# Optimization experiments

Hardware: AMD Instinct MI355X
Metric: run time of the kernel (lower is better)

The kernel has to match this reference:

```python
import jax, jax.numpy as jnp
import numpy as np

N, E, F, EF, D, G = 25000, 100000, 32, 8, 64, 1000


def setup_inputs() -> dict:
    key = jax.random.key(0)
    ks = jax.random.split(key, 32)
    p = lambda k, shape: (jax.random.normal(k, shape, jnp.float32) * 0.05)
    inp = {
        "x": jax.random.normal(ks[0], (N, F), jnp.float32),
        "edge_index": jax.random.randint(ks[1], (2, E), 0, N, jnp.int64 if jax.config.jax_enable_x64 else jnp.int32),
        "edge_attr": jax.random.uniform(ks[2], (E, EF), jnp.float32),
        "batch": jnp.sort(jax.random.randint(ks[3], (N,), 0, G, jnp.int32)),
        # lin0
        "W0": p(ks[4], (F, D)), "b0": p(ks[5], (D,)),
        # edge MLP: Linear(EF, D) -> ReLU -> Linear(D, D*D)
        "We1": p(ks[6], (EF, D)), "be1": p(ks[7], (D,)),
        "We2": p(ks[8], (D, D * D)), "be2": p(ks[9], (D * D,)),
        # NNConv root weight + bias
        "Wroot": p(ks[10], (D, D)), "bconv": p(ks[11], (D,)),
        # GRU (single layer): gate order r, z, n
        "Wi": p(ks[12], (3 * D, D)), "Wh": p(ks[13], (3 * D, D)),
        "bi": p(ks[14], (3 * D,)), "bh": p(ks[15], (3 * D,)),
        # heads
        "W11": p(ks[16], (D, D)), "b11": p(ks[17], (D,)),
        "W12": p(ks[18], (D, D)), "b12": p(ks[19], (D,)),
        "W13": p(ks[20], (D, 1)), "b13": p(ks[21], (1,)),
        "W21": p(ks[22], (D, D)), "b21": p(ks[23], (D,)),
        "W22": p(ks[24], (D, D)), "b22": p(ks[25], (D,)),
        "W23": p(ks[26], (D, 1)), "b23": p(ks[27], (1,)),
    }
    return inp


def reference(x, edge_index, edge_attr, batch,
              W0, b0, We1, be1, We2, be2, Wroot, bconv,
              Wi, Wh, bi, bh,
              W11, b11, W12, b12, W13, b13,
              W21, b21, W22, b22, W23, b23):
    src, dst = edge_index[0], edge_index[1]
    # lin0 + relu
    x1 = jax.nn.relu(x @ W0 + b0)                      # [N, D]
    h = x1                                              # GRU hidden init
    # NNConv: dynamic per-edge weight via edge MLP
    ew = (jax.nn.relu(edge_attr @ We1 + be1) @ We2 + be2).reshape(E, D, D)
    msg = jnp.einsum('ei,eio->eo', x1[src], ew)        # per-edge matmul
    agg = jax.ops.segment_sum(msg, dst, num_segments=N)
    x2 = jax.nn.relu(x1 @ Wroot + agg + bconv)         # [N, D]
    # GRU single step (torch gate order: r, z, n)
    gi = x2 @ Wi.T + bi
    gh = h @ Wh.T + bh
    r = jax.nn.sigmoid(gi[:, :D] + gh[:, :D])
    z = jax.nn.sigmoid(gi[:, D:2 * D] + gh[:, D:2 * D])
    n = jnp.tanh(gi[:, 2 * D:] + r * gh[:, 2 * D:])
    hn = (1.0 - z) * n + z * h                          # [N, D]
    # graph pooling (scatter_add over batch)
    pooled = jax.ops.segment_sum(hn, batch, num_segments=G)  # [G, D]
    # two MLP heads
    x_1 = jax.nn.relu(pooled @ W11 + b11)
    x_1 = jax.nn.relu(x_1 @ W12 + b12)
    x_1 = x_1 @ W13 + b13
    x_2 = jax.nn.relu(pooled @ W21 + b21)
    x_2 = jax.nn.relu(x_2 @ W22 + b22)
    x_2 = x_2 @ W23 + b23
    return jnp.concatenate([x_1, x_2], axis=1)          # [G, 2]
```

## Files before the change

kernel.cpp:

```cpp
#include <hip/hip_runtime.h>
#include <hip/hip_bf16.h>

#define NN 25000
#define NE 100000
#define FIN 32
#define DD 64
#define NG 1000

typedef unsigned short u16;
typedef __attribute__((ext_vector_type(8))) short short8;
typedef __attribute__((ext_vector_type(4))) float f32x4;

__device__ __forceinline__ float b2f(u16 u) {
    union { unsigned int i; float f; } v; v.i = ((unsigned int)u) << 16; return v.f;
}
__device__ __forceinline__ u16 f2b(float f) {
    __hip_bfloat16 h = __float2bfloat16(f);
    return __builtin_bit_cast(u16, h);
}
__device__ __forceinline__ bool idx_is_i64(const int* e) {
    return (e[1] == 0) & (e[3] == 0) & (e[5] == 0) & (e[7] == 0) & (e[9] == 0);
}
__device__ __forceinline__ int ld_src(const int* e, int i, bool i64) {
    return i64 ? e[2 * i] : e[i];
}
__device__ __forceinline__ int ld_dst(const int* e, int i, bool i64) {
    return i64 ? e[2 * (NE + i)] : e[NE + i];
}

__global__ __launch_bounds__(256) void k_pre(const float* __restrict__ x,
                                             const float* __restrict__ W0,
                                             const float* __restrict__ b0,
                                             u16* __restrict__ x1b,
                                             const float* __restrict__ We2,
                                             const float* __restrict__ be2,
                                             float* __restrict__ agg,
                                             float* __restrict__ pooled,
                                             u16* __restrict__ Bt2,
                                             const float* __restrict__ Wi,
                                             const float* __restrict__ Wh,
                                             const float* __restrict__ Wroot,
                                             u16* __restrict__ Wib,
                                             u16* __restrict__ Whb,
                                             u16* __restrict__ Wrb) {
    __shared__ float sbuf[4096 + 512];
    int tid = threadIdx.x;
    if (blockIdx.x < 1563) {
        float* sW = sbuf;
        float* sx = sbuf + 4096;
        for (int i = tid; i < FIN * DD; i += 256) sW[i] = W0[i];
        int nbase = blockIdx.x * 16;
        for (int i = tid; i < 16 * FIN; i += 256) {
            int nl = i >> 5, f = i & 31;
            int n = nbase + nl;
            sx[i] = (n < NN) ? x[n * FIN + f] : 0.f;
        }
        __syncthreads();
        int lane = tid & 63, nl = tid >> 6;
        float bias = b0[lane];
        #pragma unroll
        for (int rr = 0; rr < 4; rr++) {
            int row = nl * 4 + rr;
            int n = nbase + row;
            if (n < NN) {
                float acc = bias;
                #pragma unroll
                for (int f = 0; f < FIN; f++) acc += sx[row * FIN + f] * sW[f * DD + lane];
                x1b[n * DD + lane] = f2b(fmaxf(acc, 0.f));
            }
        }
    } else if (blockIdx.x < 1628) {
        int kc = blockIdx.x - 1563;
        const float* src = (kc < 64) ? (We2 + kc * 4096) : be2;
        for (int i = tid; i < 4096; i += 256) sbuf[i] = src[i];
        __syncthreads();
        for (int m = tid; m < 4096; m += 256) {
            int f = m >> 9, ln = (m >> 3) & 63, j = m & 7;
            int s = f >> 2, c = f & 3;
            int o = c * 16 + (ln & 15);
            int rlow = s * 32 + (ln >> 4) * 8 + j;
            Bt2[kc * 4096 + m] = f2b(sbuf[rlow * 64 + o]);
        }
    } else {
        int tid0 = (blockIdx.x - 1628) * 256 + threadIdx.x;
        const int STR = 256 * 256;
        for (int i = tid0; i < NN * DD; i += STR) agg[i] = 0.f;
        for (int i = tid0; i < NG * DD; i += STR) pooled[i] = 0.f;
        for (int i = tid0; i < 12288; i += STR) {
            int fr = i >> 9, lane = (i >> 3) & 63, j = i & 7;
            int c = fr >> 1, kcx = fr & 1;
            int row = c * 16 + (lane & 15);
            int col = kcx * 32 + (lane >> 4) * 8 + j;
            Wib[i] = f2b(Wi[row * 64 + col]);
            Whb[i] = f2b(Wh[row * 64 + col]);
        }
        for (int i = tid0; i < 4096; i += STR) {
            int fr = i >> 9, lane = (i >> 3) & 63, j = i & 7;
            int c = fr >> 1, kcx = fr & 1;
            int row = c * 16 + (lane & 15);
            int col = kcx * 32 + (lane >> 4) * 8 + j;
            Wrb[i] = f2b(Wroot[col * 64 + row]);
        }
    }
}

__global__ __launch_bounds__(512, 4) void k_msg(const float* __restrict__ ea,
                                                const int* __restrict__ eidx,
                                                const float* __restrict__ We1,
                                                const float* __restrict__ be1,
                                                const u16* __restrict__ x1b,
                                                const u16* __restrict__ Bt2,
                                                float* __restrict__ agg) {
    __shared__ __align__(16) u16 sX[128 * 72];
    __shared__ __align__(16) float sT[65 * 128];
    __shared__ float sWe1[8 * 64];
    __shared__ float sbe1[64];
    __shared__ int sDst[128];
    const int tid = threadIdx.x;
    const int lane = tid & 63, wv = tid >> 6;
    const int ll = lane & 15, quad = lane >> 4;
    const int rh = wv >> 2, cq = wv & 3;
    const int e0 = blockIdx.x * 128;
    const bool i64 = idx_is_i64(eidx);

    if (tid < 512) sWe1[tid] = We1[tid];
    if (tid < 64) sbe1[tid] = be1[tid];
    if (tid < 128) {
        sDst[tid] = (e0 + tid < NE) ? ld_dst(eidx, e0 + tid, i64) : 0;
        sT[64 * 128 + tid] = 1.0f;
    }

    const int el4 = tid >> 2, seg = tid & 3;
    const int eg4 = e0 + el4;
    {
        if (eg4 < NE) {
            int sv = ld_src(eidx, eg4, i64);
            const u16* xr = x1b + sv * 64 + seg * 16;
            *(uint4*)&sX[el4 * 72 + seg * 16]     = *(const uint4*)(xr);
            *(uint4*)&sX[el4 * 72 + seg * 16 + 8] = *(const uint4*)(xr + 8);
        } else {
            uint4 z = make_uint4(0, 0, 0, 0);
            *(uint4*)&sX[el4 * 72 + seg * 16]     = z;
            *(uint4*)&sX[el4 * 72 + seg * 16 + 8] = z;
        }
    }
    float eav[8];
    if (eg4 < NE) {
        f32x4 v0 = *(const f32x4*)(ea + eg4 * 8);
        f32x4 v1 = *(const f32x4*)(ea + eg4 * 8 + 4);
        #pragma unroll
        for (int f = 0; f < 4; f++) { eav[f] = v0[f]; eav[4 + f] = v1[f]; }
    } else {
        #pragma unroll
        for (int f = 0; f < 8; f++) eav[f] = 0.f;
    }
    __syncthreads();

    {
        int k0 = seg * 16;
        for (int kk = 0; kk < 16; kk++) {
            int k = k0 + kk;
            float acc = sbe1[k];
            #pragma unroll
            for (int f = 0; f < 8; f++) acc += eav[f] * sWe1[f * 64 + k];
            sT[k * 128 + el4] = (eg4 < NE) ? fmaxf(acc, 0.f) : 0.f;
        }
    }
    __syncthreads();

    short8 xa[4][2];
    #pragma unroll
    for (int rt = 0; rt < 4; rt++)
        #pragma unroll
        for (int s = 0; s < 2; s++)
            xa[rt][s] = *(const short8*)&sX[(rh * 64 + rt * 16 + ll) * 72 + s * 32 + quad * 8];

    f32x4 msg[4];
    #pragma unroll
    for (int rt = 0; rt < 4; rt++) msg[rt] = (f32x4){0.f, 0.f, 0.f, 0.f};

    const u16* gB0 = Bt2 + (0 * 4 + cq) * 512 + lane * 8;
    const u16* gB1 = Bt2 + (1 * 4 + cq) * 512 + lane * 8;
    const f32x4 zero = (f32x4){0.f, 0.f, 0.f, 0.f};
    const int tkoff = rh * 64 + quad * 4;

    short8 c00 = *(const short8*)(gB0);
    short8 c01 = *(const short8*)(gB1);
    short8 c10 = *(const short8*)(gB0 + 4096);
    short8 c11 = *(const short8*)(gB1 + 4096);
    f32x4 tkA[4], tkB[4];
    #pragma unroll
    for (int rt = 0; rt < 4; rt++)
        tkA[rt] = *(const f32x4*)&sT[tkoff + rt * 16];

    for (int kc = 0; kc < 62; kc += 2) {
        short8 n00 = *(const short8*)(gB0 + (kc + 2) * 4096);
        short8 n01 = *(const short8*)(gB1 + (kc + 2) * 4096);
        short8 n10 = *(const short8*)(gB0 + (kc + 3) * 4096);
        short8 n11 = *(const short8*)(gB1 + (kc + 3) * 4096);
        #pragma unroll
        for (int rt = 0; rt < 4; rt++)
            tkB[rt] = *(const f32x4*)&sT[(kc + 1) * 128 + tkoff + rt * 16];
        #pragma unroll
        for (int rt = 0; rt < 4; rt++) {
            f32x4 q0 = __builtin_amdgcn_mfma_f32_16x16x32_bf16(xa[rt][0], c00, zero, 0, 0, 0);
            f32x4 q1 = __builtin_amdgcn_mfma_f32_16x16x32_bf16(xa[rt][1], c01, zero, 0, 0, 0);
            msg[rt] += tkA[rt] * q0;
            msg[rt] += tkA[rt] * q1;
        }
        #pragma unroll
        for (int rt = 0; rt < 4; rt++)
            tkA[rt] = *(const f32x4*)&sT[(kc + 2) * 128 + tkoff + rt * 16];
        #pragma unroll
        for (int rt = 0; rt < 4; rt++) {
            f32x4 q0 = __builtin_amdgcn_mfma_f32_16x16x32_bf16(xa[rt][0], c10, zero, 0, 0, 0);
            f32x4 q1 = __builtin_amdgcn_mfma_f32_16x16x32_bf16(xa[rt][1], c11, zero, 0, 0, 0);
            msg[rt] += tkB[rt] * q0;
            msg[rt] += tkB[rt] * q1;
        }
        c00 = n00; c01 = n01; c10 = n10; c11 = n11;
    }
    {
        short8 n00 = *(const short8*)(gB0 + 64 * 4096);
        short8 n01 = *(const short8*)(gB1 + 64 * 4096);
        #pragma unroll
        for (int rt = 0; rt < 4; rt++)
            tkB[rt] = *(const f32x4*)&sT[63 * 128 + tkoff + rt * 16];
        #pragma unroll
        for (int rt = 0; rt < 4; rt++) {
            f32x4 q0 = __builtin_amdgcn_mfma_f32_16x16x32_bf16(xa[rt][0], c00, zero, 0, 0, 0);
            f32x4 q1 = __builtin_amdgcn_mfma_f32_16x16x32_bf16(xa[rt][1], c01, zero, 0, 0, 0);
            msg[rt] += tkA[rt] * q0;
            msg[rt] += tkA[rt] * q1;
        }
        #pragma unroll
        for (int rt = 0; rt < 4; rt++)
            tkA[rt] = *(const f32x4*)&sT[64 * 128 + tkoff + rt * 16];
        #pragma unroll
        for (int rt = 0; rt < 4; rt++) {
            f32x4 q0 = __builtin_amdgcn_mfma_f32_16x16x32_bf16(xa[rt][0], c10, zero, 0, 0, 0);
            f32x4 q1 = __builtin_amdgcn_mfma_f32_16x16x32_bf16(xa[rt][1], c11, zero, 0, 0, 0);
            msg[rt] += tkB[rt] * q0;
            msg[rt] += tkB[rt] * q1;
        }
        #pragma unroll
        for (int rt = 0; rt < 4; rt++) {
            f32x4 q0 = __builtin_amdgcn_mfma_f32_16x16x32_bf16(xa[rt][0], n00, zero, 0, 0, 0);
            f32x4 q1 = __builtin_amdgcn_mfma_f32_16x16x32_bf16(xa[rt][1], n01, zero, 0, 0, 0);
            msg[rt] += tkA[rt] * q0;
            msg[rt] += tkA[rt] * q1;
        }
    }

    #pragma unroll
    for (int rt = 0; rt < 4; rt++) {
        #pragma unroll
        for (int r = 0; r < 4; r++) {
            int el = rh * 64 + rt * 16 + quad * 4 + r;
            int eg = e0 + el;
            if (eg < NE) {
                int d = sDst[el];
                atomicAdd(&agg[d * 64 + cq * 16 + ll], msg[rt][r]);
            }
        }
    }
}

__global__ __launch_bounds__(256) void k_gru(const u16* __restrict__ x1b,
                                             const float* __restrict__ agg,
                                             const u16* __restrict__ Wib,
                                             const u16* __restrict__ Whb,
                                             const u16* __restrict__ Wrb,
                                             const float* __restrict__ bconv,
                                             const float* __restrict__ bi,
                                             const float* __restrict__ bh,
                                             const int* __restrict__ batch,
                                             float* __restrict__ pooled) {
    __shared__ __align__(16) u16 sX2[64 * 72];
    __shared__ float hbuf[64 * 65];
    __shared__ int sBatch[64];
    const int tid = threadIdx.x;
    const int lane = tid & 63, wv = tid >> 6;
    const int ll = lane & 15, quad = lane >> 4;
    const int n0 = blockIdx.x * 64;

    if (tid < 64) {
        int n = n0 + tid;
        sBatch[tid] = (n < NN) ? batch[n] : -1;
    }

    short8 ha[2];
    {
        int n = n0 + wv * 16 + ll;
        #pragma unroll
        for (int kc = 0; kc < 2; kc++) {
            if (n < NN) ha[kc] = *(const short8*)(x1b + n * 64 + kc * 32 + quad * 8);
            else        ha[kc] = (short8){0,0,0,0,0,0,0,0};
        }
    }
    f32x4 acc1[4];
    #pragma unroll
    for (int c = 0; c < 4; c++) acc1[c] = (f32x4){0.f, 0.f, 0.f, 0.f};
    #pragma unroll
    for (int kc = 0; kc < 2; kc++) {
        #pragma unroll
        for (int c = 0; c < 4; c++) {
            short8 b = *(const short8*)&Wrb[(c * 2 + kc) * 512 + lane * 8];
            acc1[c] = __builtin_amdgcn_mfma_f32_16x16x32_bf16(ha[kc], b, acc1[c], 0, 0, 0);
        }
    }
    #pragma unroll
    for (int c = 0; c < 4; c++) {
        int col = c * 16 + ll;
        float bcv = bconv[col];
        #pragma unroll
        for (int r = 0; r < 4; r++) {
            int row = wv * 16 + quad * 4 + r;
            int n = n0 + row;
            float v = 0.f;
            if (n < NN) v = fmaxf(acc1[c][r] + agg[n * 64 + col] + bcv, 0.f);
            sX2[row * 72 + col] = f2b(v);
        }
    }
    __syncthreads();

    short8 xa[2];
    #pragma unroll
    for (int kc = 0; kc < 2; kc++)
        xa[kc] = *(const short8*)&sX2[(wv * 16 + ll) * 72 + kc * 32 + quad * 8];

    f32x4 agi[12], agh[12];
    #pragma unroll
    for (int c = 0; c < 12; c++) { agi[c] = (f32x4){0.f,0.f,0.f,0.f}; agh[c] = (f32x4){0.f,0.f,0.f,0.f}; }
    #pragma unroll
    for (int kc = 0; kc < 2; kc++) {
        #pragma unroll
        for (int c = 0; c < 12; c++) {
            short8 bi8 = *(const short8*)&Wib[(c * 2 + kc) * 512 + lane * 8];
            short8 bh8 = *(const short8*)&Whb[(c * 2 + kc) * 512 + lane * 8];
            agi[c] = __builtin_amdgcn_mfma_f32_16x16x32_bf16(xa[kc], bi8, agi[c], 0, 0, 0);
            agh[c] = __builtin_amdgcn_mfma_f32_16x16x32_bf16(ha[kc], bh8, agh[c], 0, 0, 0);
        }
    }

    float hnv[4][4];
    #pragma unroll
    for (int c0 = 0; c0 < 4; c0++) {
        int d = c0 * 16 + ll;
        float bir = bi[d],        bhr = bh[d];
        float biz = bi[64 + d],   bhz = bh[64 + d];
        float bin = bi[128 + d],  bhn = bh[128 + d];
        #pragma unroll
        for (int r = 0; r < 4; r++) {
            int row = wv * 16 + quad * 4 + r;
            int n = n0 + row;
            float gir = agi[c0][r] + bir,     ghr = agh[c0][r] + bhr;
            float giz = agi[c0 + 4][r] + biz, ghz = agh[c0 + 4][r] + bhz;
            float gin = agi[c0 + 8][r] + bin, ghn = agh[c0 + 8][r] + bhn;
            float rg = 1.f / (1.f + __expf(-(gir + ghr)));
            float zg = 1.f / (1.f + __expf(-(giz + ghz)));
            float ng = tanhf(gin + rg * ghn);
            float hv = (n < NN) ? b2f(x1b[n * 64 + d]) : 0.f;
            hnv[c0][r] = (n < NN) ? ((1.f - zg) * ng + zg * hv) : 0.f;
        }
    }
    __syncthreads();

    #pragma unroll
    for (int c0 = 0; c0 < 4; c0++) {
        int d = c0 * 16 + ll;
        #pragma unroll
        for (int r = 0; r < 4; r++) {
            int row = wv * 16 + quad * 4 + r;
            hbuf[row * 65 + d] = hnv[c0][r];
        }
    }
    __syncthreads();

    {
        int d = lane;
        float sum = 0.f;
        int pb = sBatch[wv * 16];
        #pragma unroll
        for (int rr = 0; rr < 16; rr++) {
            int row = wv * 16 + rr;
            int b = sBatch[row];
            float v = hbuf[row * 65 + d];
            if (b != pb) {
                if (pb >= 0) atomicAdd(&pooled[pb * 64 + d], sum);
                sum = v; pb = b;
            } else {
                sum += v;
            }
        }
        if (pb >= 0) atomicAdd(&pooled[pb * 64 + d], sum);
    }
}

__global__ __launch_bounds__(256) void k_heads(const float* __restrict__ pooled,
                                               const float* __restrict__ W11, const float* __restrict__ b11,
                                               const float* __restrict__ W12, const float* __restrict__ b12,
                                               const float* __restrict__ W13, const float* __restrict__ b13,
                                               const float* __restrict__ W21, const float* __restrict__ b21,
                                               const float* __restrict__ W22, const float* __restrict__ b22,
                                               const float* __restrict__ W23, const float* __restrict__ b23,
                                               float* __restrict__ out) {
    __shared__ float sV[4][64];
    __shared__ float sA[4][64];
    int tid = threadIdx.x, lane = tid & 63, wv = tid >> 6;
    int g = blockIdx.x * 4 + wv;
    if (g >= NG) return;
    float p = pooled[g * 64 + lane];
    sV[wv][lane] = p;
    float y[2];
    const float* W1s[2] = {W11, W21}; const float* b1s[2] = {b11, b21};
    const float* W2s[2] = {W12, W22}; const float* b2s[2] = {b12, b22};
    const float* W3s[2] = {W13, W23}; const float* b3s[2] = {b13, b23};
    #pragma unroll
    for (int hd = 0; hd < 2; hd++) {
        float a = b1s[hd][lane];
        #pragma unroll 8
        for (int i = 0; i < 64; i++) a += sV[wv][i] * W1s[hd][i * 64 + lane];
        a = fmaxf(a, 0.f);
        sA[wv][lane] = a;
        float a2 = b2s[hd][lane];
        #pragma unroll 8
        for (int i = 0; i < 64; i++) a2 += sA[wv][i] * W2s[hd][i * 64 + lane];
        a2 = fmaxf(a2, 0.f);
        float part = a2 * W3s[hd][lane];
        #pragma unroll
        for (int m = 32; m > 0; m >>= 1) part += __shfl_xor(part, m, 64);
        y[hd] = part + b3s[hd][0];
    }
    if (lane == 0) {
        out[g * 2 + 0] = y[0];
        out[g * 2 + 1] = y[1];
    }
}

extern "C" void kernel_launch(void* const* d_in, const int* in_sizes, int n_in,
                              void* d_out, int out_size, void* d_ws, size_t ws_size,
                              hipStream_t stream) {
    const float* x     = (const float*)d_in[0];
    const int* eidx    = (const int*)d_in[1];
    const float* ea    = (const float*)d_in[2];
    const int* batch   = (const int*)d_in[3];
    const float* W0    = (const float*)d_in[4];  const float* b0    = (const float*)d_in[5];
    const float* We1   = (const float*)d_in[6];  const float* be1   = (const float*)d_in[7];
    const float* We2   = (const float*)d_in[8];  const float* be2   = (const float*)d_in[9];
    const float* Wroot = (const float*)d_in[10]; const float* bconv = (const float*)d_in[11];
    const float* Wi    = (const float*)d_in[12]; const float* Wh    = (const float*)d_in[13];
    const float* bi    = (const float*)d_in[14]; const float* bh    = (const float*)d_in[15];
    const float* W11   = (const float*)d_in[16]; const float* b11   = (const float*)d_in[17];
    const float* W12   = (const float*)d_in[18]; const float* b12   = (const float*)d_in[19];
    const float* W13   = (const float*)d_in[20]; const float* b13   = (const float*)d_in[21];
    const float* W21   = (const float*)d_in[22]; const float* b21   = (const float*)d_in[23];
    const float* W22   = (const float*)d_in[24]; const float* b22   = (const float*)d_in[25];
    const float* W23   = (const float*)d_in[26]; const float* b23   = (const float*)d_in[27];
    float* out = (float*)d_out;

    char* ws = (char*)d_ws;
    float* agg    = (float*)(ws);
    u16*   x1b    = (u16*)(ws + 6400000);
    u16*   Bt2    = (u16*)(ws + 9600000);
    float* pooled = (float*)(ws + 10132480);
    u16*   Wib    = (u16*)(ws + 10388480);
    u16*   Whb    = (u16*)(ws + 10413056);
    u16*   Wrb    = (u16*)(ws + 10437632);

    hipLaunchKernelGGL(k_pre, dim3(1884), dim3(256), 0, stream,
                       x, W0, b0, x1b, We2, be2, agg, pooled, Bt2,
                       Wi, Wh, Wroot, Wib, Whb, Wrb);
    hipLaunchKernelGGL(k_msg, dim3(782), dim3(512), 0, stream, ea, eidx, We1, be1, x1b, Bt2, agg);
    hipLaunchKernelGGL(k_gru, dim3(391), dim3(256), 0, stream, x1b, agg,
                       Wib, Whb, Wrb, bconv, bi, bh, batch, pooled);
    hipLaunchKernelGGL(k_heads, dim3(250), dim3(256), 0, stream, pooled,
                       W11, b11, W12, b12, W13, b13, W21, b21, W22, b22, W23, b23, out);
}
```

Before: 233.4 us.

## Switch to fp16 and fold edge-hidden scaling into MFMA A operand accumulation

Converts all packed operands from bf16 to fp16 and restructures the per-edge message loop. Instead of running a zero-initialised MFMA per hidden unit and then scaling its result on vector ALUs, each row's x1 fragment is scaled by the edge hidden activation with packed half multiplies, and the MFMA accumulates directly. The sT layout is permuted so one 16-byte load per k gives each lane its four edge scalars. This removes the per-k fp32 multiply-adds and the extra tkA/tkB register traffic, at the cost of fp16 range and precision risk and packed multiplies on the A operand every iteration.

```diff
diff --git a/kernel.cpp b/kernel.cpp
--- a/kernel.cpp
+++ b/kernel.cpp
@@ -1,5 +1,6 @@
 #include <hip/hip_runtime.h>
 #include <hip/hip_bf16.h>
+#include <hip/hip_fp16.h>
 
 #define NN 25000
 #define NE 100000
@@ -9,14 +10,25 @@
 
 typedef unsigned short u16;
 typedef __attribute__((ext_vector_type(8))) short short8;
+typedef __attribute__((ext_vector_type(8))) _Float16 f16x8;
 typedef __attribute__((ext_vector_type(4))) float f32x4;
 
-__device__ __forceinline__ float b2f(u16 u) {
-    union { unsigned int i; float f; } v; v.i = ((unsigned int)u) << 16; return v.f;
-}
-__device__ __forceinline__ u16 f2b(float f) {
-    __hip_bfloat16 h = __float2bfloat16(f);
+__device__ __forceinline__ u16 f2h(float f) {
+    __half h = __float2half(f);
     return __builtin_bit_cast(u16, h);
+}
+__device__ __forceinline__ float h2f(u16 u) {
+    __half h = __builtin_bit_cast(__half, u);
+    return __half2float(h);
+}
+__device__ __forceinline__ f16x8 s2h(short8 v) { return __builtin_bit_cast(f16x8, v); }
+__device__ __forceinline__ short8 scale8(short8 v, __half2 t) {
+    union { short8 s; __half2 h[4]; } u; u.s = v;
+    u.h[0] = __hmul2(u.h[0], t);
+    u.h[1] = __hmul2(u.h[1], t);
+    u.h[2] = __hmul2(u.h[2], t);
+    u.h[3] = __hmul2(u.h[3], t);
+    return u.s;
 }
 __device__ __forceinline__ bool idx_is_i64(const int* e) {
     return (e[1] == 0) & (e[3] == 0) & (e[5] == 0) & (e[7] == 0) & (e[9] == 0);
@@ -66,7 +78,7 @@
                 float acc = bias;
                 #pragma unroll
                 for (int f = 0; f < FIN; f++) acc += sx[row * FIN + f] * sW[f * DD + lane];
-                x1b[n * DD + lane] = f2b(fmaxf(acc, 0.f));
+                x1b[n * DD + lane] = f2h(fmaxf(acc, 0.f));
             }
         }
     } else if (blockIdx.x < 1628) {
@@ -79,7 +91,7 @@
             int s = f >> 2, c = f & 3;
             int o = c * 16 + (ln & 15);
             int rlow = s * 32 + (ln >> 4) * 8 + j;
-            Bt2[kc * 4096 + m] = f2b(sbuf[rlow * 64 + o]);
+            Bt2[kc * 4096 + m] = f2h(sbuf[rlow * 64 + o]);
         }
     } else {
         int tid0 = (blockIdx.x - 1628) * 256 + threadIdx.x;
@@ -91,15 +103,15 @@
             int c = fr >> 1, kcx = fr & 1;
             int row = c * 16 + (lane & 15);
             int col = kcx * 32 + (lane >> 4) * 8 + j;
-            Wib[i] = f2b(Wi[row * 64 + col]);
-            Whb[i] = f2b(Wh[row * 64 + col]);
+            Wib[i] = f2h(Wi[row * 64 + col]);
+            Whb[i] = f2h(Wh[row * 64 + col]);
         }
         for (int i = tid0; i < 4096; i += STR) {
             int fr = i >> 9, lane = (i >> 3) & 63, j = i & 7;
             int c = fr >> 1, kcx = fr & 1;
             int row = c * 16 + (lane & 15);
             int col = kcx * 32 + (lane >> 4) * 8 + j;
-            Wrb[i] = f2b(Wroot[col * 64 + row]);
+            Wrb[i] = f2h(Wroot[col * 64 + row]);
         }
     }
 }
@@ -157,13 +169,15 @@
     __syncthreads();
 
     {
+        int eh = el4 & 63;
+        const int tpos = (el4 >> 6) * 64 + (eh & 15) * 4 + (eh >> 4);
         int k0 = seg * 16;
         for (int kk = 0; kk < 16; kk++) {
             int k = k0 + kk;
             float acc = sbe1[k];
             #pragma unroll
             for (int f = 0; f < 8; f++) acc += eav[f] * sWe1[f * 64 + k];
-            sT[k * 128 + el4] = (eg4 < NE) ? fmaxf(acc, 0.f) : 0.f;
+            sT[k * 128 + tpos] = (eg4 < NE) ? fmaxf(acc, 0.f) : 0.f;
         }
     }
     __syncthreads();
@@ -175,81 +189,31 @@
         for (int s = 0; s < 2; s++)
             xa[rt][s] = *(const short8*)&sX[(rh * 64 + rt * 16 + ll) * 72 + s * 32 + quad * 8];
 
-    f32x4 msg[4];
-    #pragma unroll
-    for (int rt = 0; rt < 4; rt++) msg[rt] = (f32x4){0.f, 0.f, 0.f, 0.f};
+    f32x4 acc[4];
+    #pragma unroll
+    for (int rt = 0; rt < 4; rt++) acc[rt] = (f32x4){0.f, 0.f, 0.f, 0.f};
 
     const u16* gB0 = Bt2 + (0 * 4 + cq) * 512 + lane * 8;
     const u16* gB1 = Bt2 + (1 * 4 + cq) * 512 + lane * 8;
-    const f32x4 zero = (f32x4){0.f, 0.f, 0.f, 0.f};
-    const int tkoff = rh * 64 + quad * 4;
-
-    short8 c00 = *(const short8*)(gB0);
-    short8 c01 = *(const short8*)(gB1);
-    short8 c10 = *(const short8*)(gB0 + 4096);
-    short8 c11 = *(const short8*)(gB1 + 4096);
-    f32x4 tkA[4], tkB[4];
-    #pragma unroll
-    for (int rt = 0; rt < 4; rt++)
-        tkA[rt] = *(const f32x4*)&sT[tkoff + rt * 16];
-
-    for (int kc = 0; kc < 62; kc += 2) {
-        short8 n00 = *(const short8*)(gB0 + (kc + 2) * 4096);
-        short8 n01 = *(const short8*)(gB1 + (kc + 2) * 4096);
-        short8 n10 = *(const short8*)(gB0 + (kc + 3) * 4096);
-        short8 n11 = *(const short8*)(gB1 + (kc + 3) * 4096);
-        #pragma unroll
-        for (int rt = 0; rt < 4; rt++)
-            tkB[rt] = *(const f32x4*)&sT[(kc + 1) * 128 + tkoff + rt * 16];
+
+    short8 c0 = *(const short8*)(gB0);
+    short8 c1 = *(const short8*)(gB1);
+
+    for (int kc = 0; kc < 65; kc++) {
+        int kn = (kc < 64) ? kc + 1 : 64;
+        short8 n0 = *(const short8*)(gB0 + kn * 4096);
+        short8 n1 = *(const short8*)(gB1 + kn * 4096);
+        f32x4 tq = *(const f32x4*)&sT[kc * 128 + rh * 64 + ll * 4];
+        f16x8 b0 = s2h(c0), b1 = s2h(c1);
         #pragma unroll
         for (int rt = 0; rt < 4; rt++) {
-            f32x4 q0 = __builtin_amdgcn_mfma_f32_16x16x32_bf16(xa[rt][0], c00, zero, 0, 0, 0);
-            f32x4 q1 = __builtin_amdgcn_mfma_f32_16x16x32_bf16(xa[rt][1], c01, zero, 0, 0, 0);
-            msg[rt] += tkA[rt] * q0;
-            msg[rt] += tkA[rt] * q1;
-        }
-        #pragma unroll
-        for (int rt = 0; rt < 4; rt++)
-            tkA[rt] = *(const f32x4*)&sT[(kc + 2) * 128 + tkoff + rt * 16];
-        #pragma unroll
-        for (int rt = 0; rt < 4; rt++) {
-            f32x4 q0 = __builtin_amdgcn_mfma_f32_16x16x32_bf16(xa[rt][0], c10, zero, 0, 0, 0);
-            f32x4 q1 = __builtin_amdgcn_mfma_f32_16x16x32_bf16(xa[rt][1], c11, zero, 0, 0, 0);
-            msg[rt] += tkB[rt] * q0;
-            msg[rt] += tkB[rt] * q1;
-        }
-        c00 = n00; c01 = n01; c10 = n10; c11 = n11;
-    }
-    {
-        short8 n00 = *(const short8*)(gB0 + 64 * 4096);
-        short8 n01 = *(const short8*)(gB1 + 64 * 4096);
-        #pragma unroll
-        for (int rt = 0; rt < 4; rt++)
-            tkB[rt] = *(const f32x4*)&sT[63 * 128 + tkoff + rt * 16];
-        #pragma unroll
-        for (int rt = 0; rt < 4; rt++) {
-            f32x4 q0 = __builtin_amdgcn_mfma_f32_16x16x32_bf16(xa[rt][0], c00, zero, 0, 0, 0);
-            f32x4 q1 = __builtin_amdgcn_mfma_f32_16x16x32_bf16(xa[rt][1], c01, zero, 0, 0, 0);
-            msg[rt] += tkA[rt] * q0;
-            msg[rt] += tkA[rt] * q1;
-        }
-        #pragma unroll
-        for (int rt = 0; rt < 4; rt++)
-            tkA[rt] = *(const f32x4*)&sT[64 * 128 + tkoff + rt * 16];
-        #pragma unroll
-        for (int rt = 0; rt < 4; rt++) {
-            f32x4 q0 = __builtin_amdgcn_mfma_f32_16x16x32_bf16(xa[rt][0], c10, zero, 0, 0, 0);
-            f32x4 q1 = __builtin_amdgcn_mfma_f32_16x16x32_bf16(xa[rt][1], c11, zero, 0, 0, 0);
-            msg[rt] += tkB[rt] * q0;
-            msg[rt] += tkB[rt] * q1;
-        }
-        #pragma unroll
-        for (int rt = 0; rt < 4; rt++) {
-            f32x4 q0 = __builtin_amdgcn_mfma_f32_16x16x32_bf16(xa[rt][0], n00, zero, 0, 0, 0);
-            f32x4 q1 = __builtin_amdgcn_mfma_f32_16x16x32_bf16(xa[rt][1], n01, zero, 0, 0, 0);
-            msg[rt] += tkA[rt] * q0;
-            msg[rt] += tkA[rt] * q1;
-        }
+            __half2 th = __float2half2_rn(tq[rt]);
+            f16x8 a0 = s2h(scale8(xa[rt][0], th));
+            f16x8 a1 = s2h(scale8(xa[rt][1], th));
+            acc[rt] = __builtin_amdgcn_mfma_f32_16x16x32_f16(a0, b0, acc[rt], 0, 0, 0);
+            acc[rt] = __builtin_amdgcn_mfma_f32_16x16x32_f16(a1, b1, acc[rt], 0, 0, 0);
+        }
+        c0 = n0; c1 = n1;
     }
 
     #pragma unroll
@@ -260,7 +224,7 @@
             int eg = e0 + el;
             if (eg < NE) {
                 int d = sDst[el];
-                atomicAdd(&agg[d * 64 + cq * 16 + ll], msg[rt][r]);
+                atomicAdd(&agg[d * 64 + cq * 16 + ll], acc[rt][r]);
             }
         }
     }
@@ -306,7 +270,7 @@
         #pragma unroll
         for (int c = 0; c < 4; c++) {
             short8 b = *(const short8*)&Wrb[(c * 2 + kc) * 512 + lane * 8];
-            acc1[c] = __builtin_amdgcn_mfma_f32_16x16x32_bf16(ha[kc], b, acc1[c], 0, 0, 0);
+            acc1[c] = __builtin_amdgcn_mfma_f32_16x16x32_f16(s2h(ha[kc]), s2h(b), acc1[c], 0, 0, 0);
         }
     }
     #pragma unroll
@@ -319,7 +283,7 @@
             int n = n0 + row;
             float v = 0.f;
             if (n < NN) v = fmaxf(acc1[c][r] + agg[n * 64 + col] + bcv, 0.f);
-            sX2[row * 72 + col] = f2b(v);
+            sX2[row * 72 + col] = f2h(v);
         }
     }
     __syncthreads();
@@ -338,8 +302,8 @@
         for (int c = 0; c < 12; c++) {
             short8 bi8 = *(const short8*)&Wib[(c * 2 + kc) * 512 + lane * 8];
             short8 bh8 = *(const short8*)&Whb[(c * 2 + kc) * 512 + lane * 8];
-            agi[c] = __builtin_amdgcn_mfma_f32_16x16x32_bf16(xa[kc], bi8, agi[c], 0, 0, 0);
-            agh[c] = __builtin_amdgcn_mfma_f32_16x16x32_bf16(ha[kc], bh8, agh[c], 0, 0, 0);
+            agi[c] = __builtin_amdgcn_mfma_f32_16x16x32_f16(s2h(xa[kc]), s2h(bi8), agi[c], 0, 0, 0);
+            agh[c] = __builtin_amdgcn_mfma_f32_16x16x32_f16(s2h(ha[kc]), s2h(bh8), agh[c], 0, 0, 0);
         }
     }
 
@@ -360,7 +324,7 @@
             float rg = 1.f / (1.f + __expf(-(gir + ghr)));
             float zg = 1.f / (1.f + __expf(-(giz + ghz)));
             float ng = tanhf(gin + rg * ghn);
-            float hv = (n < NN) ? b2f(x1b[n * 64 + d]) : 0.f;
+            float hv = (n < NN) ? h2f(x1b[n * 64 + d]) : 0.f;
             hnv[c0][r] = (n < NN) ? ((1.f - zg) * ng + zg * hv) : 0.f;
         }
     }
```

Measured after the change: 227.0 us. 2.7% less time.
